# Kernel tuning notes

Measured on AMD Instinct MI355X. Metric: run time of the kernel, lower is better.

The kernel has to match this reference:

```python
import jax, jax.numpy as jnp
import numpy as np

B, S, D = 2, 2048, 2048
H = 16
NOPE, ROPE, VH = 128, 64, 128
QR, KVR = 512, 512
EPS = 1e-6


def _rmsnorm(x, w):
    return x * jax.lax.rsqrt(jnp.mean(x * x, axis=-1, keepdims=True) + EPS) * w


def _rope(t, freqs_cis):
    # t: (B, h, S, ROPE); freqs_cis: (S, ROPE//2, 2) as (cos, sin)
    b, h, s, d = t.shape
    t2 = t.reshape(b, h, s, d // 2, 2)
    cos = freqs_cis[:, :, 0][None, None]  # (1,1,S,ROPE//2)
    sin = freqs_cis[:, :, 1][None, None]
    x0, x1 = t2[..., 0], t2[..., 1]
    r0 = x0 * cos - x1 * sin
    r1 = x0 * sin + x1 * cos
    return jnp.stack([r0, r1], axis=-1).reshape(b, h, s, d)


def setup_inputs() -> dict:
    key = jax.random.key(0)
    ks = jax.random.split(key, 11)
    def init(k, out_dim, in_dim):
        return jax.random.normal(k, (out_dim, in_dim), jnp.float32) * (1.0 / np.sqrt(in_dim))
    x = jax.random.normal(ks[0], (B, S, D), jnp.float32)
    half = ROPE // 2
    inv = 1.0 / (10000.0 ** (np.arange(half, dtype=np.float64) / half))
    ang = np.outer(np.arange(S), inv)
    freqs_cis = jnp.asarray(np.stack([np.cos(ang), np.sin(ang)], axis=-1), jnp.float32)  # (S, half, 2)
    mask = jnp.ones((S, S), dtype=bool)  # unused (is_causal=True in original)
    return {
        "x": x,
        "mask": mask,
        "freqs_cis": freqs_cis,
        "w_cq": init(ks[1], QR, D),
        "w_qnorm": jnp.ones((QR,), jnp.float32),
        "w_dqn": init(ks[2], H * NOPE, QR),
        "w_dqr": init(ks[3], H * ROPE, QR),
        "w_ckv": init(ks[4], KVR, D),
        "w_kvnorm": jnp.ones((KVR,), jnp.float32),
        "w_dkn": init(ks[5], H * NOPE, KVR),
        "w_dv": init(ks[6], H * VH, KVR),
        "w_krope": init(ks[7], ROPE, D),
        "w_proj": init(ks[8], D, H * VH),
    }


def reference(x, mask, freqs_cis, w_cq, w_qnorm, w_dqn, w_dqr, w_ckv, w_kvnorm, w_dkn, w_dv, w_krope, w_proj):
    b, s, _ = x.shape
    # Q path: compress -> RMSNorm -> decompress (nope, rope)
    cq = jnp.einsum('bsd,rd->bsr', x, w_cq)
    nq = _rmsnorm(cq, w_qnorm)
    q_nope = jnp.einsum('bsr,er->bse', nq, w_dqn).reshape(b, s, H, NOPE).transpose(0, 2, 1, 3)
    q_rope = jnp.einsum('bsr,er->bse', nq, w_dqr).reshape(b, s, H, ROPE).transpose(0, 2, 1, 3)
    # KV path
    ckv = jnp.einsum('bsd,rd->bsr', x, w_ckv)
    nkv = _rmsnorm(ckv, w_kvnorm)
    k_nope = jnp.einsum('bsr,er->bse', nkv, w_dkn).reshape(b, s, H, NOPE).transpose(0, 2, 1, 3)
    value = jnp.einsum('bsr,er->bse', nkv, w_dv).reshape(b, s, H, VH).transpose(0, 2, 1, 3)
    # shared single-head rope key, scaled by 1/num_heads
    k_rope = jnp.einsum('bsd,ed->bse', x, w_krope).reshape(b, s, 1, ROPE).transpose(0, 2, 1, 3) / H
    # partial RoPE
    q_rope = _rope(q_rope, freqs_cis)
    k_rope = _rope(k_rope, freqs_cis)
    # recombine nope|rope
    q = jnp.concatenate([q_nope, q_rope], axis=-1)  # (B,H,S,NOPE+ROPE)
    k = jnp.concatenate([k_nope, jnp.broadcast_to(k_rope, (b, H, s, ROPE))], axis=-1)
    # causal SDPA
    scale = 1.0 / np.sqrt(NOPE + ROPE)
    scores = jnp.einsum('bhqd,bhkd->bhqk', q, k) * scale
    causal = jnp.tril(jnp.ones((s, s), dtype=bool))
    scores = jnp.where(causal[None, None], scores, -jnp.inf)
    attn = jax.nn.softmax(scores, axis=-1)
    out = jnp.einsum('bhqk,bhkv->bhqv', attn, value)  # (B,H,S,VH)
    out = out.transpose(0, 2, 1, 3).reshape(b, s, H * VH)
    return jnp.einsum('bse,de->bsd', out, w_proj)
```

## Files before the change

kernel.cpp:

```cpp
#include <hip/hip_runtime.h>
#include <hip/hip_bf16.h>


typedef __attribute__((ext_vector_type(8))) short s8v;
typedef __attribute__((ext_vector_type(4))) float f4v;

#define DEV static __device__ __forceinline__

DEV ushort f2b(float f) {
  __hip_bfloat16 h = __float2bfloat16(f);
  return *reinterpret_cast<ushort*>(&h);
}
DEV float b2f(ushort u) {
  __hip_bfloat16 h = *reinterpret_cast<__hip_bfloat16*>(&u);
  return __bfloat162float(h);
}
DEV f4v mfma16(s8v a, s8v b, f4v c) {
  return __builtin_amdgcn_mfma_f32_16x16x32_bf16(a, b, c, 0, 0, 0);
}
DEV void gload16(const ushort* g, ushort* l) {
  __builtin_amdgcn_global_load_lds((const __attribute__((address_space(1))) void*)g,
                                   (__attribute__((address_space(3))) void*)l, 16, 0, 0);
}

__global__ void cast_f2b_kernel(const float* __restrict__ src, ushort* __restrict__ dst, int n4) {
  int i = blockIdx.x * 256 + threadIdx.x;
  if (i >= n4) return;
  float4 v = reinterpret_cast<const float4*>(src)[i];
  ushort4 o;
  o.x = f2b(v.x); o.y = f2b(v.y); o.z = f2b(v.z); o.w = f2b(v.w);
  reinterpret_cast<ushort4*>(dst)[i] = o;
}

__global__ void fill_zero_kernel(ushort* __restrict__ dst, int n8) {
  int i = blockIdx.x * 256 + threadIdx.x;
  if (i >= n8) return;
  reinterpret_cast<uint4*>(dst)[i] = uint4{0u, 0u, 0u, 0u};
}

template <bool BF16OUT>
__global__ __launch_bounds__(256) void gemm_bt(const ushort* __restrict__ A,
                                               const ushort* __restrict__ B,
                                               void* __restrict__ C,
                                               int M, int N, int K) {
  __shared__ ushort a_lds[2][128 * 32];
  __shared__ ushort b_lds[2][128 * 32];
  const int tid = threadIdx.x;
  const int lane = tid & 63, wv = tid >> 6;
  const int wm = wv >> 1, wn = wv & 1;
  const int l15 = lane & 15, l4 = lane >> 4;
  const int row0 = blockIdx.x * 128, col0 = blockIdx.y * 128;
  const int srow = lane >> 2;
  const int scol = (lane & 3) * 8;

  f4v acc[4][4];
#pragma unroll
  for (int i = 0; i < 4; ++i)
#pragma unroll
    for (int j = 0; j < 4; ++j) acc[i][j] = f4v{0.f, 0.f, 0.f, 0.f};

  auto stage = [&](int k0, int bsel) {
#pragma unroll
    for (int i = 0; i < 2; ++i) {
      int s = wv * 2 + i;
      gload16(&A[(size_t)(row0 + s * 16 + srow) * K + k0 + scol], &a_lds[bsel][s * 512]);
      gload16(&B[(size_t)(col0 + s * 16 + srow) * K + k0 + scol], &b_lds[bsel][s * 512]);
    }
  };

  stage(0, 0);
  int cur = 0;
  for (int k0 = 0; k0 < K; k0 += 32) {
    __syncthreads();
    if (k0 + 32 < K) stage(k0 + 32, cur ^ 1);
    s8v af[4], bfr[4];
#pragma unroll
    for (int mi = 0; mi < 4; ++mi)
      af[mi] = *reinterpret_cast<const s8v*>(&a_lds[cur][(wm * 64 + mi * 16 + l15) * 32 + 8 * l4]);
#pragma unroll
    for (int ni = 0; ni < 4; ++ni)
      bfr[ni] = *reinterpret_cast<const s8v*>(&b_lds[cur][(wn * 64 + ni * 16 + l15) * 32 + 8 * l4]);
#pragma unroll
    for (int mi = 0; mi < 4; ++mi)
#pragma unroll
      for (int ni = 0; ni < 4; ++ni) acc[mi][ni] = mfma16(af[mi], bfr[ni], acc[mi][ni]);
    cur ^= 1;
  }

#pragma unroll
  for (int mi = 0; mi < 4; ++mi)
#pragma unroll
    for (int ni = 0; ni < 4; ++ni)
#pragma unroll
      for (int j = 0; j < 4; ++j) {
        int r = row0 + wm * 64 + mi * 16 + l4 * 4 + j;
        int cl = col0 + wn * 64 + ni * 16 + l15;
        if (BF16OUT)
          reinterpret_cast<ushort*>(C)[(size_t)r * N + cl] = f2b(acc[mi][ni][j]);
        else
          reinterpret_cast<float*>(C)[(size_t)r * N + cl] = acc[mi][ni][j];
      }
}

__global__ __launch_bounds__(256) void norm_rope1_kernel(
    const float* __restrict__ g1, const float* __restrict__ wq, const float* __restrict__ wkv,
    const float* __restrict__ freqs, ushort* __restrict__ nq, ushort* __restrict__ nkv,
    ushort* __restrict__ kro) {
  const int m = blockIdx.x;
  const int s = m & 2047;
  const int tid = threadIdx.x;
  __shared__ float red[4];
  const float* row = g1 + (size_t)m * 1152;

  float v0 = row[tid], v1 = row[tid + 256];
  float ss = v0 * v0 + v1 * v1;
#pragma unroll
  for (int off = 32; off > 0; off >>= 1) ss += __shfl_down(ss, off);
  if ((tid & 63) == 0) red[tid >> 6] = ss;
  __syncthreads();
  float r = rsqrtf((red[0] + red[1] + red[2] + red[3]) * (1.0f / 512.0f) + 1e-6f);
  nq[(size_t)m * 512 + tid] = f2b(v0 * r * wq[tid]);
  nq[(size_t)m * 512 + tid + 256] = f2b(v1 * r * wq[tid + 256]);

  float u0 = row[512 + tid], u1 = row[512 + tid + 256];
  float ss2 = u0 * u0 + u1 * u1;
#pragma unroll
  for (int off = 32; off > 0; off >>= 1) ss2 += __shfl_down(ss2, off);
  __syncthreads();
  if ((tid & 63) == 0) red[tid >> 6] = ss2;
  __syncthreads();
  float r2 = rsqrtf((red[0] + red[1] + red[2] + red[3]) * (1.0f / 512.0f) + 1e-6f);
  nkv[(size_t)m * 512 + tid] = f2b(u0 * r2 * wkv[tid]);
  nkv[(size_t)m * 512 + tid + 256] = f2b(u1 * r2 * wkv[tid + 256]);

  if (tid < 32) {
    float x0 = row[1024 + 2 * tid], x1 = row[1024 + 2 * tid + 1];
    float c = freqs[s * 64 + 2 * tid], sn = freqs[s * 64 + 2 * tid + 1];
    kro[(size_t)m * 64 + 2 * tid] = f2b((x0 * c - x1 * sn) * (1.0f / 16.0f));
    kro[(size_t)m * 64 + 2 * tid + 1] = f2b((x0 * sn + x1 * c) * (1.0f / 16.0f));
  }
}

__global__ void rope_q_kernel(ushort* __restrict__ g2q, const float* __restrict__ freqs) {
  int idx = blockIdx.x * 256 + threadIdx.x;
  int m = idx >> 9;
  int rem = idx & 511;
  int h = rem >> 5, j = rem & 31;
  int s = m & 2047;
  size_t base = (size_t)m * 3072 + 2048 + h * 64 + 2 * j;
  ushort2 pr = *reinterpret_cast<ushort2*>(&g2q[base]);
  float x0 = b2f(pr.x), x1 = b2f(pr.y);
  float c = freqs[s * 64 + 2 * j], sn = freqs[s * 64 + 2 * j + 1];
  ushort2 o;
  o.x = f2b(x0 * c - x1 * sn);
  o.y = f2b(x0 * sn + x1 * c);
  *reinterpret_cast<ushort2*>(&g2q[base]) = o;
}

__global__ __launch_bounds__(256) void transpose_v_kernel(const ushort* __restrict__ g2kv,
                                                          ushort* __restrict__ vT) {
  int blk = blockIdx.x;
  int bh = blk >> 6;
  int rem = blk & 63;
  int st = rem >> 1, dt = rem & 1;
  int b = bh >> 4, h = bh & 15;
  __shared__ ushort t[64][72];
  int tid = threadIdx.x;
#pragma unroll
  for (int it = 0; it < 2; ++it) {
    int c = tid + it * 256;
    int sl = c >> 3, cc = (c & 7) * 8;
    *reinterpret_cast<uint4*>(&t[sl][cc]) = *reinterpret_cast<const uint4*>(
        &g2kv[(size_t)(b * 2048 + st * 64 + sl) * 4096 + 2048 + h * 128 + dt * 64 + cc]);
  }
  __syncthreads();
#pragma unroll
  for (int it = 0; it < 2; ++it) {
    int c = tid + it * 256;
    int dl = c >> 3, cc = (c & 7) * 8;
    ushort tmp[8];
#pragma unroll
    for (int e = 0; e < 8; ++e) tmp[e] = t[cc + e][dl];
    *reinterpret_cast<uint4*>(&vT[(size_t)(bh * 128 + dt * 64 + dl) * 2048 + st * 64 + cc]) =
        *reinterpret_cast<uint4*>(tmp);
  }
}

__global__ __launch_bounds__(512) void attn_kernel(const ushort* __restrict__ q,
                                                   const ushort* __restrict__ knope,
                                                   const ushort* __restrict__ kro,
                                                   const ushort* __restrict__ vT,
                                                   ushort* __restrict__ out) {
  const int lid = blockIdx.x;
  const int bh = lid & 31;
  const int qt = 15 - (lid >> 5);
  const int b = bh >> 4, h = bh & 15;
  const int tid = threadIdx.x, lane = tid & 63, w = tid >> 6;
  const int l15 = lane & 15, l4 = lane >> 4;

  __shared__ ushort kbuf[2][64 * 192];
  __shared__ ushort vbuf[2][128 * 64];
  __shared__ ushort p_lds[8][16][72];

  s8v qf[6];
  {
    const size_t qbase = (size_t)(b * 2048 + qt * 128 + w * 16 + l15) * 3072;
#pragma unroll
    for (int kc = 0; kc < 4; ++kc)
      qf[kc] = *reinterpret_cast<const s8v*>(&q[qbase + h * 128 + kc * 32 + 8 * l4]);
#pragma unroll
    for (int kc = 4; kc < 6; ++kc)
      qf[kc] = *reinterpret_cast<const s8v*>(&q[qbase + 2048 + h * 64 + (kc - 4) * 32 + 8 * l4]);
  }

  f4v oacc[8];
#pragma unroll
  for (int i = 0; i < 8; ++i) oacc[i] = f4v{0.f, 0.f, 0.f, 0.f};
  float m_r[4] = {-INFINITY, -INFINITY, -INFINITY, -INFINITY};
  float l_r[4] = {0.f, 0.f, 0.f, 0.f};
  const float scale = 0.07216878364870323f;
  const int nkt = 2 * qt + 2;
  const int kbase = b * 2048;

  auto stage = [&](int kt, int bsel) {
    const int krow0 = kbase + kt * 64;
#pragma unroll
    for (int i = 0; i < 3; ++i) {
      int s = w * 3 + i;
      int p = s * 1024 + lane * 16;
      int row = p / 384;
      int col = ((p ^ ((row & 7) << 4)) - row * 384) >> 1;
      const ushort* src = (col < 128)
          ? &knope[(size_t)(krow0 + row) * 4096 + h * 128 + col]
          : &kro[(size_t)(krow0 + row) * 64 + (col - 128)];
      gload16(src, &kbuf[bsel][s * 512]);
    }
#pragma unroll
    for (int i = 0; i < 2; ++i) {
      int s = w * 2 + i;
      int p = s * 1024 + lane * 16;
      int d = p >> 7;
      int key = ((p ^ ((d & 7) << 4)) & 127) >> 1;
      gload16(&vT[(size_t)(bh * 128 + d) * 2048 + kt * 64 + key], &vbuf[bsel][s * 512]);
    }
  };

  stage(0, 0);
  int cur = 0;
  for (int kt = 0; kt < nkt; ++kt) {
    __syncthreads();
    if (kt + 1 < nkt) stage(kt + 1, cur ^ 1);
    const char* kb = (const char*)kbuf[cur];
    const char* vb = (const char*)vbuf[cur];

    f4v sacc[4];
#pragma unroll
    for (int nb = 0; nb < 4; ++nb) {
      sacc[nb] = f4v{0.f, 0.f, 0.f, 0.f};
      const int row = nb * 16 + l15;
      const int sw = (row & 7) << 4;
#pragma unroll
      for (int kc = 0; kc < 6; ++kc) {
        s8v bfr = *reinterpret_cast<const s8v*>(kb + row * 384 + ((kc * 64 + l4 * 16) ^ sw));
        sacc[nb] = mfma16(qf[kc], bfr, sacc[nb]);
      }
    }
    const int qrow0 = qt * 128 + w * 16 + l4 * 4;
#pragma unroll
    for (int nb = 0; nb < 4; ++nb) {
      int key = kt * 64 + nb * 16 + l15;
#pragma unroll
      for (int j = 0; j < 4; ++j) {
        float sv = sacc[nb][j] * scale;
        if (kt >= 2 * qt && key > qrow0 + j) sv = -INFINITY;
        sacc[nb][j] = sv;
      }
    }
    float mx[4];
#pragma unroll
    for (int j = 0; j < 4; ++j)
      mx[j] = fmaxf(fmaxf(sacc[0][j], sacc[1][j]), fmaxf(sacc[2][j], sacc[3][j]));
#pragma unroll
    for (int off = 1; off < 16; off <<= 1)
#pragma unroll
      for (int j = 0; j < 4; ++j) mx[j] = fmaxf(mx[j], __shfl_xor(mx[j], off));
    float al[4], rs[4];
#pragma unroll
    for (int j = 0; j < 4; ++j) {
      float mnew = fmaxf(m_r[j], mx[j]);
      al[j] = __expf(m_r[j] - mnew);
      m_r[j] = mnew;
      rs[j] = 0.f;
    }
#pragma unroll
    for (int nb = 0; nb < 4; ++nb)
#pragma unroll
      for (int j = 0; j < 4; ++j) {
        float p = __expf(sacc[nb][j] - m_r[j]);
        sacc[nb][j] = p;
        rs[j] += p;
      }
#pragma unroll
    for (int off = 1; off < 16; off <<= 1)
#pragma unroll
      for (int j = 0; j < 4; ++j) rs[j] += __shfl_xor(rs[j], off);
#pragma unroll
    for (int j = 0; j < 4; ++j) l_r[j] = l_r[j] * al[j] + rs[j];
#pragma unroll
    for (int nb = 0; nb < 4; ++nb)
#pragma unroll
      for (int j = 0; j < 4; ++j)
        p_lds[w][l4 * 4 + j][nb * 16 + l15] = f2b(sacc[nb][j]);
#pragma unroll
    for (int nv = 0; nv < 8; ++nv)
#pragma unroll
      for (int j = 0; j < 4; ++j) oacc[nv][j] *= al[j];
#pragma unroll
    for (int kc2 = 0; kc2 < 2; ++kc2) {
      s8v pf = *reinterpret_cast<const s8v*>(&p_lds[w][l15][kc2 * 32 + 8 * l4]);
#pragma unroll
      for (int nv = 0; nv < 8; ++nv) {
        const int d = nv * 16 + l15;
        s8v vf = *reinterpret_cast<const s8v*>(vb + d * 128 + ((kc2 * 64 + l4 * 16) ^ ((d & 7) << 4)));
        oacc[nv] = mfma16(pf, vf, oacc[nv]);
      }
    }
    cur ^= 1;
  }

#pragma unroll
  for (int j = 0; j < 4; ++j) {
    float inv = 1.0f / l_r[j];
    int m = b * 2048 + qt * 128 + w * 16 + l4 * 4 + j;
#pragma unroll
    for (int nv = 0; nv < 8; ++nv)
      out[(size_t)m * 2048 + h * 128 + nv * 16 + l15] = f2b(oacc[nv][j] * inv);
  }
}

extern "C" void kernel_launch(void* const* d_in, const int* in_sizes, int n_in,
                              void* d_out, int out_size, void* d_ws, size_t ws_size,
                              hipStream_t stream) {
  const float* x       = (const float*)d_in[0];
  const float* freqs   = (const float*)d_in[2];
  const float* w_cq    = (const float*)d_in[3];
  const float* w_qnorm = (const float*)d_in[4];
  const float* w_dqn   = (const float*)d_in[5];
  const float* w_dqr   = (const float*)d_in[6];
  const float* w_ckv   = (const float*)d_in[7];
  const float* w_kvnorm= (const float*)d_in[8];
  const float* w_dkn   = (const float*)d_in[9];
  const float* w_dv    = (const float*)d_in[10];
  const float* w_krope = (const float*)d_in[11];
  const float* w_proj  = (const float*)d_in[12];
  float* out = (float*)d_out;

  char* ws = (char*)d_ws;
  const size_t MB = 1ull << 20;
  ushort* g2kv = (ushort*)(ws + 0);
  float*  g1   = (float*) (ws + 0);
  ushort* g2q  = (ushort*)(ws + 32 * MB);
  ushort* xbf  = (ushort*)(ws + 32 * MB);
  ushort* w1   = (ushort*)(ws + 48 * MB);
  ushort* vT   = (ushort*)(ws + 56 * MB);
  ushort* nq   = (ushort*)(ws + 56 * MB);
  ushort* nkv  = (ushort*)(ws + 60 * MB);
  ushort* w2q  = (ushort*)(ws + 64 * MB);
  ushort* w2kv = (ushort*)(ws + 67 * MB);
  ushort* att  = (ushort*)(ws + 72 * MB);
  ushort* wpj  = (ushort*)(ws + 88 * MB);
  ushort* kro  = (ushort*)(ws + 96 * MB);

  auto cast = [&](const float* s, ushort* d, int n) {
    cast_f2b_kernel<<<(n / 4 + 255) / 256, 256, 0, stream>>>(s, d, n / 4);
  };
  cast(x, xbf, 4096 * 2048);
  cast(w_cq, w1, 512 * 2048);
  cast(w_ckv, w1 + 512 * 2048, 512 * 2048);
  cast(w_krope, w1 + 1024 * 2048, 64 * 2048);
  fill_zero_kernel<<<64, 256, 0, stream>>>(w1 + 1088 * 2048, 64 * 2048 / 8);
  cast(w_dqn, w2q, 2048 * 512);
  cast(w_dqr, w2q + 2048 * 512, 1024 * 512);
  cast(w_dkn, w2kv, 2048 * 512);
  cast(w_dv, w2kv + 2048 * 512, 2048 * 512);
  cast(w_proj, wpj, 2048 * 2048);

  gemm_bt<false><<<dim3(32, 9), 256, 0, stream>>>(xbf, w1, g1, 4096, 1152, 2048);
  norm_rope1_kernel<<<4096, 256, 0, stream>>>(g1, w_qnorm, w_kvnorm, freqs, nq, nkv, kro);
  gemm_bt<true><<<dim3(32, 24), 256, 0, stream>>>(nq, w2q, g2q, 4096, 3072, 512);
  gemm_bt<true><<<dim3(32, 32), 256, 0, stream>>>(nkv, w2kv, g2kv, 4096, 4096, 512);
  rope_q_kernel<<<8192, 256, 0, stream>>>(g2q, freqs);
  transpose_v_kernel<<<2048, 256, 0, stream>>>(g2kv, vT);
  attn_kernel<<<512, 512, 0, stream>>>(g2q, g2kv, kro, vT, att);
  gemm_bt<false><<<dim3(32, 16), 256, 0, stream>>>(att, wpj, out, 4096, 2048, 2048);
}
```

Before: 420.5 us.

## Merge launches, read V directly from global, and add lazy softmax rescaling

The ten cast kernels become one table-driven launch, and the two decompress GEMMs become a single dual-grid kernel. RoPE-Q and the V transpose are merged into one launch. In attention, V is no longer staged through LDS but loaded straight from global memory, and the softmax switches to exp2 with a folded scale. The running max and the output are only rescaled when the max grows by more than 8, and setprio hints are added around the MFMA sections. Reading V from global with strided per-row loads may add memory latency in exchange for lower LDS use and higher occupancy.

```diff
diff --git a/kernel.cpp b/kernel.cpp
--- a/kernel.cpp
+++ b/kernel.cpp
@@ -23,35 +23,38 @@
                                    (__attribute__((address_space(3))) void*)l, 16, 0, 0);
 }
 
-__global__ void cast_f2b_kernel(const float* __restrict__ src, ushort* __restrict__ dst, int n4) {
-  int i = blockIdx.x * 256 + threadIdx.x;
-  if (i >= n4) return;
-  float4 v = reinterpret_cast<const float4*>(src)[i];
+struct CastSeg { const float* src; ushort* dst; int n4; int blk0; };
+struct CastTab { CastSeg seg[10]; };
+
+__global__ __launch_bounds__(256) void cast_all_kernel(CastTab t) {
+  int b = blockIdx.x;
+  int si = 0;
+#pragma unroll
+  for (int i = 1; i < 10; ++i) si = (b >= t.seg[i].blk0) ? i : si;
+  int i4 = (b - t.seg[si].blk0) * 256 + threadIdx.x;
+  if (i4 >= t.seg[si].n4) return;
   ushort4 o;
-  o.x = f2b(v.x); o.y = f2b(v.y); o.z = f2b(v.z); o.w = f2b(v.w);
-  reinterpret_cast<ushort4*>(dst)[i] = o;
-}
-
-__global__ void fill_zero_kernel(ushort* __restrict__ dst, int n8) {
-  int i = blockIdx.x * 256 + threadIdx.x;
-  if (i >= n8) return;
-  reinterpret_cast<uint4*>(dst)[i] = uint4{0u, 0u, 0u, 0u};
+  if (t.seg[si].src) {
+    float4 v = reinterpret_cast<const float4*>(t.seg[si].src)[i4];
+    o.x = f2b(v.x); o.y = f2b(v.y); o.z = f2b(v.z); o.w = f2b(v.w);
+  } else {
+    o = ushort4{0, 0, 0, 0};
+  }
+  reinterpret_cast<ushort4*>(t.seg[si].dst)[i4] = o;
 }
 
 template <bool BF16OUT>
-__global__ __launch_bounds__(256) void gemm_bt(const ushort* __restrict__ A,
-                                               const ushort* __restrict__ B,
-                                               void* __restrict__ C,
-                                               int M, int N, int K) {
-  __shared__ ushort a_lds[2][128 * 32];
-  __shared__ ushort b_lds[2][128 * 32];
+DEV void gemm_core(const ushort* __restrict__ A, const ushort* __restrict__ B,
+                   void* __restrict__ C, int N, int K, int row0, int col0,
+                   ushort* a_lds0, ushort* a_lds1, ushort* b_lds0, ushort* b_lds1) {
   const int tid = threadIdx.x;
   const int lane = tid & 63, wv = tid >> 6;
   const int wm = wv >> 1, wn = wv & 1;
   const int l15 = lane & 15, l4 = lane >> 4;
-  const int row0 = blockIdx.x * 128, col0 = blockIdx.y * 128;
   const int srow = lane >> 2;
   const int scol = (lane & 3) * 8;
+  ushort* a_lds[2] = {a_lds0, a_lds1};
+  ushort* b_lds[2] = {b_lds0, b_lds1};
 
   f4v acc[4][4];
 #pragma unroll
@@ -100,6 +103,28 @@
         else
           reinterpret_cast<float*>(C)[(size_t)r * N + cl] = acc[mi][ni][j];
       }
+}
+
+template <bool BF16OUT>
+__global__ __launch_bounds__(256) void gemm_bt(const ushort* __restrict__ A,
+                                               const ushort* __restrict__ B,
+                                               void* __restrict__ C, int N, int K) {
+  __shared__ ushort a0[128 * 32], a1[128 * 32], b0[128 * 32], b1[128 * 32];
+  gemm_core<BF16OUT>(A, B, C, N, K, blockIdx.x * 128, blockIdx.y * 128, a0, a1, b0, b1);
+}
+
+__global__ __launch_bounds__(256) void gemm2_dual(const ushort* __restrict__ nq,
+                                                  const ushort* __restrict__ w2q,
+                                                  ushort* __restrict__ g2q,
+                                                  const ushort* __restrict__ nkv,
+                                                  const ushort* __restrict__ w2kv,
+                                                  ushort* __restrict__ g2kv) {
+  __shared__ ushort a0[128 * 32], a1[128 * 32], b0[128 * 32], b1[128 * 32];
+  int by = blockIdx.y;
+  if (by < 24)
+    gemm_core<true>(nq, w2q, g2q, 3072, 512, blockIdx.x * 128, by * 128, a0, a1, b0, b1);
+  else
+    gemm_core<true>(nkv, w2kv, g2kv, 4096, 512, blockIdx.x * 128, (by - 24) * 128, a0, a1, b0, b1);
 }
 
 __global__ __launch_bounds__(256) void norm_rope1_kernel(
@@ -141,56 +166,58 @@
   }
 }
 
-__global__ void rope_q_kernel(ushort* __restrict__ g2q, const float* __restrict__ freqs) {
-  int idx = blockIdx.x * 256 + threadIdx.x;
-  int m = idx >> 9;
-  int rem = idx & 511;
-  int h = rem >> 5, j = rem & 31;
-  int s = m & 2047;
-  size_t base = (size_t)m * 3072 + 2048 + h * 64 + 2 * j;
-  ushort2 pr = *reinterpret_cast<ushort2*>(&g2q[base]);
-  float x0 = b2f(pr.x), x1 = b2f(pr.y);
-  float c = freqs[s * 64 + 2 * j], sn = freqs[s * 64 + 2 * j + 1];
-  ushort2 o;
-  o.x = f2b(x0 * c - x1 * sn);
-  o.y = f2b(x0 * sn + x1 * c);
-  *reinterpret_cast<ushort2*>(&g2q[base]) = o;
-}
-
-__global__ __launch_bounds__(256) void transpose_v_kernel(const ushort* __restrict__ g2kv,
-                                                          ushort* __restrict__ vT) {
-  int blk = blockIdx.x;
-  int bh = blk >> 6;
-  int rem = blk & 63;
-  int st = rem >> 1, dt = rem & 1;
-  int b = bh >> 4, h = bh & 15;
-  __shared__ ushort t[64][72];
-  int tid = threadIdx.x;
-#pragma unroll
-  for (int it = 0; it < 2; ++it) {
-    int c = tid + it * 256;
-    int sl = c >> 3, cc = (c & 7) * 8;
-    *reinterpret_cast<uint4*>(&t[sl][cc]) = *reinterpret_cast<const uint4*>(
-        &g2kv[(size_t)(b * 2048 + st * 64 + sl) * 4096 + 2048 + h * 128 + dt * 64 + cc]);
-  }
-  __syncthreads();
-#pragma unroll
-  for (int it = 0; it < 2; ++it) {
-    int c = tid + it * 256;
-    int dl = c >> 3, cc = (c & 7) * 8;
-    ushort tmp[8];
-#pragma unroll
-    for (int e = 0; e < 8; ++e) tmp[e] = t[cc + e][dl];
-    *reinterpret_cast<uint4*>(&vT[(size_t)(bh * 128 + dt * 64 + dl) * 2048 + st * 64 + cc]) =
-        *reinterpret_cast<uint4*>(tmp);
-  }
-}
-
-__global__ __launch_bounds__(512) void attn_kernel(const ushort* __restrict__ q,
-                                                   const ushort* __restrict__ knope,
-                                                   const ushort* __restrict__ kro,
-                                                   const ushort* __restrict__ vT,
-                                                   ushort* __restrict__ out) {
+__global__ __launch_bounds__(256) void misc_fused_kernel(ushort* __restrict__ g2q,
+                                                         const float* __restrict__ freqs,
+                                                         const ushort* __restrict__ g2kv,
+                                                         ushort* __restrict__ vT) {
+  const int tid = threadIdx.x;
+  if (blockIdx.x < 2048) {
+    int blk = blockIdx.x;
+    int bh = blk >> 6;
+    int rem = blk & 63;
+    int st = rem >> 1, dt = rem & 1;
+    int b = bh >> 4, h = bh & 15;
+    __shared__ ushort t[64][72];
+#pragma unroll
+    for (int it = 0; it < 2; ++it) {
+      int c = tid + it * 256;
+      int sl = c >> 3, cc = (c & 7) * 8;
+      *reinterpret_cast<uint4*>(&t[sl][cc]) = *reinterpret_cast<const uint4*>(
+          &g2kv[(size_t)(b * 2048 + st * 64 + sl) * 4096 + 2048 + h * 128 + dt * 64 + cc]);
+    }
+    __syncthreads();
+#pragma unroll
+    for (int it = 0; it < 2; ++it) {
+      int c = tid + it * 256;
+      int dl = c >> 3, cc = (c & 7) * 8;
+      ushort tmp[8];
+#pragma unroll
+      for (int e = 0; e < 8; ++e) tmp[e] = t[cc + e][dl];
+      *reinterpret_cast<uint4*>(&vT[(size_t)(bh * 128 + dt * 64 + dl) * 2048 + st * 64 + cc]) =
+          *reinterpret_cast<uint4*>(tmp);
+    }
+  } else {
+    int idx = (blockIdx.x - 2048) * 256 + tid;
+    int m = idx >> 9;
+    int rem = idx & 511;
+    int h = rem >> 5, j = rem & 31;
+    int s = m & 2047;
+    size_t base = (size_t)m * 3072 + 2048 + h * 64 + 2 * j;
+    ushort2 pr = *reinterpret_cast<ushort2*>(&g2q[base]);
+    float x0 = b2f(pr.x), x1 = b2f(pr.y);
+    float c = freqs[s * 64 + 2 * j], sn = freqs[s * 64 + 2 * j + 1];
+    ushort2 o;
+    o.x = f2b(x0 * c - x1 * sn);
+    o.y = f2b(x0 * sn + x1 * c);
+    *reinterpret_cast<ushort2*>(&g2q[base]) = o;
+  }
+}
+
+__global__ __launch_bounds__(512, 4) void attn_kernel(const ushort* __restrict__ q,
+                                                      const ushort* __restrict__ knope,
+                                                      const ushort* __restrict__ kro,
+                                                      const ushort* __restrict__ vT,
+                                                      ushort* __restrict__ out) {
   const int lid = blockIdx.x;
   const int bh = lid & 31;
   const int qt = 15 - (lid >> 5);
@@ -199,7 +226,6 @@
   const int l15 = lane & 15, l4 = lane >> 4;
 
   __shared__ ushort kbuf[2][64 * 192];
-  __shared__ ushort vbuf[2][128 * 64];
   __shared__ ushort p_lds[8][16][72];
 
   s8v qf[6];
@@ -218,9 +244,10 @@
   for (int i = 0; i < 8; ++i) oacc[i] = f4v{0.f, 0.f, 0.f, 0.f};
   float m_r[4] = {-INFINITY, -INFINITY, -INFINITY, -INFINITY};
   float l_r[4] = {0.f, 0.f, 0.f, 0.f};
-  const float scale = 0.07216878364870323f;
+  const float sc2 = 0.07216878364870323f * 1.44269504f;
   const int nkt = 2 * qt + 2;
   const int kbase = b * 2048;
+  const ushort* vbh = vT + (size_t)bh * 128 * 2048;
 
   auto stage = [&](int kt, int bsel) {
     const int krow0 = kbase + kt * 64;
@@ -235,14 +262,6 @@
           : &kro[(size_t)(krow0 + row) * 64 + (col - 128)];
       gload16(src, &kbuf[bsel][s * 512]);
     }
-#pragma unroll
-    for (int i = 0; i < 2; ++i) {
-      int s = w * 2 + i;
-      int p = s * 1024 + lane * 16;
-      int d = p >> 7;
-      int key = ((p ^ ((d & 7) << 4)) & 127) >> 1;
-      gload16(&vT[(size_t)(bh * 128 + d) * 2048 + kt * 64 + key], &vbuf[bsel][s * 512]);
-    }
   };
 
   stage(0, 0);
@@ -251,9 +270,9 @@
     __syncthreads();
     if (kt + 1 < nkt) stage(kt + 1, cur ^ 1);
     const char* kb = (const char*)kbuf[cur];
-    const char* vb = (const char*)vbuf[cur];
 
     f4v sacc[4];
+    __builtin_amdgcn_s_setprio(1);
 #pragma unroll
     for (int nb = 0; nb < 4; ++nb) {
       sacc[nb] = f4v{0.f, 0.f, 0.f, 0.f};
@@ -265,13 +284,15 @@
         sacc[nb] = mfma16(qf[kc], bfr, sacc[nb]);
       }
     }
+    __builtin_amdgcn_s_setprio(0);
+
     const int qrow0 = qt * 128 + w * 16 + l4 * 4;
 #pragma unroll
     for (int nb = 0; nb < 4; ++nb) {
       int key = kt * 64 + nb * 16 + l15;
 #pragma unroll
       for (int j = 0; j < 4; ++j) {
-        float sv = sacc[nb][j] * scale;
+        float sv = sacc[nb][j] * sc2;
         if (kt >= 2 * qt && key > qrow0 + j) sv = -INFINITY;
         sacc[nb][j] = sv;
       }
@@ -284,19 +305,29 @@
     for (int off = 1; off < 16; off <<= 1)
 #pragma unroll
       for (int j = 0; j < 4; ++j) mx[j] = fmaxf(mx[j], __shfl_xor(mx[j], off));
-    float al[4], rs[4];
-#pragma unroll
-    for (int j = 0; j < 4; ++j) {
-      float mnew = fmaxf(m_r[j], mx[j]);
-      al[j] = __expf(m_r[j] - mnew);
-      m_r[j] = mnew;
-      rs[j] = 0.f;
-    }
+
+    float need = fmaxf(fmaxf(mx[0] - m_r[0], mx[1] - m_r[1]),
+                       fmaxf(mx[2] - m_r[2], mx[3] - m_r[3]));
+    if (!__all(need <= 8.0f)) {
+      float al[4];
+#pragma unroll
+      for (int j = 0; j < 4; ++j) {
+        float mnew = fmaxf(m_r[j], mx[j]);
+        al[j] = exp2f(m_r[j] - mnew);
+        m_r[j] = mnew;
+        l_r[j] *= al[j];
+      }
+#pragma unroll
+      for (int nv = 0; nv < 8; ++nv)
+#pragma unroll
+        for (int j = 0; j < 4; ++j) oacc[nv][j] *= al[j];
+    }
+    float rs[4] = {0.f, 0.f, 0.f, 0.f};
 #pragma unroll
     for (int nb = 0; nb < 4; ++nb)
 #pragma unroll
       for (int j = 0; j < 4; ++j) {
-        float p = __expf(sacc[nb][j] - m_r[j]);
+        float p = exp2f(sacc[nb][j] - m_r[j]);
         sacc[nb][j] = p;
         rs[j] += p;
       }
@@ -305,26 +336,27 @@
 #pragma unroll
       for (int j = 0; j < 4; ++j) rs[j] += __shfl_xor(rs[j], off);
 #pragma unroll
-    for (int j = 0; j < 4; ++j) l_r[j] = l_r[j] * al[j] + rs[j];
+    for (int j = 0; j < 4; ++j) l_r[j] += rs[j];
 #pragma unroll
     for (int nb = 0; nb < 4; ++nb)
 #pragma unroll
       for (int j = 0; j < 4; ++j)
         p_lds[w][l4 * 4 + j][nb * 16 + l15] = f2b(sacc[nb][j]);
-#pragma unroll
-    for (int nv = 0; nv < 8; ++nv)
-#pragma unroll
-      for (int j = 0; j < 4; ++j) oacc[nv][j] *= al[j];
-#pragma unroll
+
+    const ushort* vbase = vbh + kt * 64;
+    __builtin_amdgcn_s_setprio(1);
+#pragma unroll 1
     for (int kc2 = 0; kc2 < 2; ++kc2) {
       s8v pf = *reinterpret_cast<const s8v*>(&p_lds[w][l15][kc2 * 32 + 8 * l4]);
-#pragma unroll
-      for (int nv = 0; nv < 8; ++nv) {
-        const int d = nv * 16 + l15;
-        s8v vf = *reinterpret_cast<const s8v*>(vb + d * 128 + ((kc2 * 64 + l4 * 16) ^ ((d & 7) << 4)));
-        oacc[nv] = mfma16(pf, vf, oacc[nv]);
-      }
-    }
+      s8v vf[8];
+#pragma unroll
+      for (int nv = 0; nv < 8; ++nv)
+        vf[nv] = *reinterpret_cast<const s8v*>(
+            &vbase[(size_t)(nv * 16 + l15) * 2048 + kc2 * 32 + 8 * l4]);
+#pragma unroll
+      for (int nv = 0; nv < 8; ++nv) oacc[nv] = mfma16(pf, vf[nv], oacc[nv]);
+    }
+    __builtin_amdgcn_s_setprio(0);
     cur ^= 1;
   }
 
@@ -371,26 +403,27 @@
   ushort* wpj  = (ushort*)(ws + 88 * MB);
   ushort* kro  = (ushort*)(ws + 96 * MB);
 
-  auto cast = [&](const float* s, ushort* d, int n) {
-    cast_f2b_kernel<<<(n / 4 + 255) / 256, 256, 0, stream>>>(s, d, n / 4);
-  };
-  cast(x, xbf, 4096 * 2048);
-  cast(w_cq, w1, 512 * 2048);
-  cast(w_ckv, w1 + 512 * 2048, 512 * 2048);
-  cast(w_krope, w1 + 1024 * 2048, 64 * 2048);
-  fill_zero_kernel<<<64, 256, 0, stream>>>(w1 + 1088 * 2048, 64 * 2048 / 8);
-  cast(w_dqn, w2q, 2048 * 512);
-  cast(w_dqr, w2q + 2048 * 512, 1024 * 512);
-  cast(w_dkn, w2kv, 2048 * 512);
-  cast(w_dv, w2kv + 2048 * 512, 2048 * 512);
-  cast(w_proj, wpj, 2048 * 2048);
-
-  gemm_bt<false><<<dim3(32, 9), 256, 0, stream>>>(xbf, w1, g1, 4096, 1152, 2048);
+  CastTab t;
+  const float* srcs[10] = {x, w_cq, w_ckv, w_krope, nullptr,
+                           w_dqn, w_dqr, w_dkn, w_dv, w_proj};
+  ushort* dsts[10] = {xbf, w1, w1 + 512 * 2048, w1 + 1024 * 2048, w1 + 1088 * 2048,
+                      w2q, w2q + 2048 * 512, w2kv, w2kv + 2048 * 512, wpj};
+  int ns[10] = {4096 * 2048, 512 * 2048, 512 * 2048, 64 * 2048, 64 * 2048,
+                2048 * 512, 1024 * 512, 2048 * 512, 2048 * 512, 2048 * 2048};
+  int blk = 0;
+  for (int i = 0; i < 10; ++i) {
+    t.seg[i].src = srcs[i];
+    t.seg[i].dst = dsts[i];
+    t.seg[i].n4 = ns[i] / 4;
+    t.seg[i].blk0 = blk;
+    blk += (ns[i] / 4 + 255) / 256;
+  }
+  cast_all_kernel<<<blk, 256, 0, stream>>>(t);
+
+  gemm_bt<false><<<dim3(32, 9), 256, 0, stream>>>(xbf, w1, g1, 1152, 2048);
   norm_rope1_kernel<<<4096, 256, 0, stream>>>(g1, w_qnorm, w_kvnorm, freqs, nq, nkv, kro);
-  gemm_bt<true><<<dim3(32, 24), 256, 0, stream>>>(nq, w2q, g2q, 4096, 3072, 512);
-  gemm_bt<true><<<dim3(32, 32), 256, 0, stream>>>(nkv, w2kv, g2kv, 4096, 4096, 512);
-  rope_q_kernel<<<8192, 256, 0, stream>>>(g2q, freqs);
-  transpose_v_kernel<<<2048, 256, 0, stream>>>(g2kv, vT);
+  gemm2_dual<<<dim3(32, 56), 256, 0, stream>>>(nq, w2q, g2q, nkv, w2kv, g2kv);
+  misc_fused_kernel<<<2048 + 8192, 256, 0, stream>>>(g2q, freqs, g2kv, vT);
   attn_kernel<<<512, 512, 0, stream>>>(g2q, g2kv, kro, vT, att);
-  gemm_bt<false><<<dim3(32, 16), 256, 0, stream>>>(att, wpj, out, 4096, 2048, 2048);
-}
+  gemm_bt<false><<<dim3(32, 16), 256, 0, stream>>>(att, wpj, out, 2048, 2048);
+}
```

After: 573.9 us. +36.5%, slower.
